# Kernel tuning notes

Hardware: AMD Instinct MI355X
Metric: run time of the kernel (lower is better)

The kernel has to match this reference:

```python
import jax, jax.numpy as jnp
import numpy as np

EMBED_DIM = 2048
NUM_HEADS = 16
NUM_KV_HEADS = 4
KEY_DIM = EMBED_DIM // NUM_HEADS  # 128
B, S = 2, 2048


def setup_inputs() -> dict:
    key = jax.random.key(0)
    ks = jax.random.split(key, 8)
    kv_dim = KEY_DIM * NUM_KV_HEADS
    sc_in = 1.0 / np.sqrt(EMBED_DIM)
    return {
        "query": jax.random.normal(ks[0], (B, S, EMBED_DIM), jnp.float32),
        "key": jax.random.normal(ks[1], (B, S, EMBED_DIM), jnp.float32),
        "value": jax.random.normal(ks[2], (B, S, EMBED_DIM), jnp.float32),
        "mask": jnp.ones((B, S), jnp.float32),
        "Wq": jax.random.normal(ks[3], (EMBED_DIM, EMBED_DIM), jnp.float32) * sc_in,
        "Wk": jax.random.normal(ks[4], (EMBED_DIM, kv_dim), jnp.float32) * sc_in,
        "Wv": jax.random.normal(ks[5], (EMBED_DIM, kv_dim), jnp.float32) * sc_in,
        "Wo": jax.random.normal(ks[6], (EMBED_DIM, EMBED_DIM), jnp.float32) * sc_in,
    }


def reference(query, key, value, mask, Wq, Wk, Wv, Wo):
    b, sq, _ = query.shape
    skv = key.shape[1]
    scale = 1.0 / float(KEY_DIM) ** 0.5
    # projections (no bias)
    q = (query @ Wq).reshape(b, sq, NUM_HEADS, KEY_DIM).transpose(0, 2, 1, 3)      # [B,H,Sq,D]
    k = (key @ Wk).reshape(b, skv, NUM_KV_HEADS, KEY_DIM).transpose(0, 2, 1, 3)    # [B,Hkv,Skv,D]
    v = (value @ Wv).reshape(b, skv, NUM_KV_HEADS, KEY_DIM).transpose(0, 2, 1, 3)  # [B,Hkv,Skv,D]
    n_rep = NUM_HEADS // NUM_KV_HEADS
    k_rep = jnp.repeat(k, n_rep, axis=1)  # [B,H,Skv,D]
    v_rep = jnp.repeat(v, n_rep, axis=1)  # [B,H,Skv,D]
    scores = jnp.einsum("bhqd,bhkd->bhqk", q, k_rep) * scale  # [B,H,Sq,Skv]
    scores = scores + (1.0 - mask[:, None, None, :].astype(scores.dtype)) * -1e9
    attn = jax.nn.softmax(scores, axis=-1)
    out = jnp.einsum("bhqk,bhkd->bhqd", attn, v_rep)  # [B,H,Sq,D]
    out = out.transpose(0, 2, 1, 3).reshape(b, sq, EMBED_DIM)
    return out @ Wo
```

## Files before the change

kernel.cpp:

```cpp
#include <hip/hip_runtime.h>
#include <hip/hip_bf16.h>

#define B_    2
#define S_    2048
#define E_    2048
#define H_    16
#define HKV_  4
#define D_    128
#define NTOK  4096
#define KVDIM 512

typedef __bf16 bf16x8 __attribute__((ext_vector_type(8)));
typedef __bf16 bf16x4 __attribute__((ext_vector_type(4)));
typedef float  f32x4  __attribute__((ext_vector_type(4)));

__device__ __forceinline__ void async_copy16(const void* g, void* l) {
  __builtin_amdgcn_global_load_lds(
      (const __attribute__((address_space(1))) unsigned int*)g,
      (__attribute__((address_space(3))) unsigned int*)l, 16, 0, 0);
}

__global__ __launch_bounds__(256) void transpose_all(
    const float* __restrict__ Wq, const float* __restrict__ Wk,
    const float* __restrict__ Wv, const float* __restrict__ Wo,
    __bf16* __restrict__ WTq, __bf16* __restrict__ WTk,
    __bf16* __restrict__ WTv, __bf16* __restrict__ WoT) {
  const float* in;
  __bf16* out;
  int C;
  switch (blockIdx.z) {
    case 0:  in = Wq; out = WTq; C = E_;   break;
    case 1:  in = Wk; out = WTk; C = KVDIM; break;
    case 2:  in = Wv; out = WTv; C = KVDIM; break;
    default: in = Wo; out = WoT; C = E_;   break;
  }
  const int c0 = blockIdx.x * 32;
  if (c0 >= C) return;
  const int r0 = blockIdx.y * 64;
  __shared__ float t[32][65];
  const int lr = threadIdx.x >> 2;
  const int lc = (threadIdx.x & 3) * 8;
  const float* ip = in + (size_t)(r0 + lr) * C + c0 + lc;
  const f32x4 a0 = *(const f32x4*)ip;
  const f32x4 a1 = *(const f32x4*)(ip + 4);
#pragma unroll
  for (int j = 0; j < 4; ++j) t[lc + j][lr] = a0[j];
#pragma unroll
  for (int j = 0; j < 4; ++j) t[lc + 4 + j][lr] = a1[j];
  __syncthreads();
  const int oc = threadIdx.x >> 3;
  const int orr = (threadIdx.x & 7) * 8;
  bf16x8 v;
#pragma unroll
  for (int j = 0; j < 8; ++j) v[j] = (__bf16)t[oc][orr + j];
  *(bf16x8*)(out + (size_t)(c0 + oc) * E_ + r0 + orr) = v;
}

__global__ __launch_bounds__(256) void convert_q(const float* __restrict__ in,
                                                 __bf16* __restrict__ ob) {
  const size_t i = ((size_t)blockIdx.x * 256 + threadIdx.x) * 8;
  const f32x4 a0 = *(const f32x4*)(in + i);
  const f32x4 a1 = *(const f32x4*)(in + i + 4);
  bf16x8 v;
#pragma unroll
  for (int j = 0; j < 4; ++j) { v[j] = (__bf16)a0[j]; v[4 + j] = (__bf16)a1[j]; }
  *(bf16x8*)(ob + i) = v;
}

__global__ __launch_bounds__(512, 1) void gemm_pipe(
    const __bf16* __restrict__ A, const __bf16* __restrict__ Bt,
    float* __restrict__ Cf, __bf16* __restrict__ Cb, int M, int N, int K,
    int epi) {
  __shared__ __align__(16) __bf16 lds[2 * 24576];

  const int n0 = blockIdx.x * 256;
  const int m0 = blockIdx.y * 128;
  const int tid = threadIdx.x;
  const int w = tid >> 6;
  const int lane = tid & 63;
  const int quad = lane >> 4;
  const int l16 = lane & 15;
  const int wm = w >> 2;
  const int wn = w & 3;
  const int lr = lane >> 3;
  const int ls = lane & 7;

  const __bf16* pa[2];
  const __bf16* pb[4];
#pragma unroll
  for (int r = 0; r < 2; ++r) {
    const int row = r * 64 + w * 8 + lr;
    pa[r] = A + (size_t)(m0 + row) * K + ((ls ^ (row & 7)) * 8);
  }
#pragma unroll
  for (int r = 0; r < 4; ++r) {
    const int row = r * 64 + w * 8 + lr;
    pb[r] = Bt + (size_t)(n0 + row) * K + ((ls ^ (row & 7)) * 8);
  }

  auto stageA = [&](int bufi) {
    __bf16* base = lds + bufi * 24576;
#pragma unroll
    for (int r = 0; r < 2; ++r) {
      async_copy16(pa[r], base + (size_t)(r * 64 + w * 8) * 64);
      pa[r] += 64;
    }
  };
  auto stageB = [&](int bufi) {
    __bf16* base = lds + bufi * 24576 + 8192;
#pragma unroll
    for (int r = 0; r < 4; ++r) {
      async_copy16(pb[r], base + (size_t)(r * 64 + w * 8) * 64);
      pb[r] += 64;
    }
  };

  f32x4 acc[4][4] = {};
  const int NT = K >> 6;
  const int xr = l16 & 7;

  stageA(0);
  stageB(0);
  stageB(1);
  asm volatile("s_waitcnt vmcnt(4)" ::: "memory");
  __builtin_amdgcn_s_barrier();

  for (int t = 0; t < NT; ++t) {
    const __bf16* lA = lds + (t & 1) * 24576;
    const __bf16* lB = lA + 8192;

    bf16x8 af[2][2], bfr[4][2];
#pragma unroll
    for (int f = 0; f < 2; ++f) {
      const int rowb = (wm * 64 + f * 16 + l16) * 64;
#pragma unroll
      for (int ks = 0; ks < 2; ++ks)
        af[f][ks] = *(const bf16x8*)&lA[rowb + (((ks * 4 + quad) ^ xr) * 8)];
    }
#pragma unroll
    for (int g = 0; g < 4; ++g) {
      const int rowb = (wn * 64 + g * 16 + l16) * 64;
#pragma unroll
      for (int ks = 0; ks < 2; ++ks)
        bfr[g][ks] = *(const bf16x8*)&lB[rowb + (((ks * 4 + quad) ^ xr) * 8)];
    }
    if (t + 1 < NT) stageA((t + 1) & 1);
    __builtin_amdgcn_s_barrier();
    asm volatile("s_waitcnt lgkmcnt(0)" ::: "memory");
    __builtin_amdgcn_sched_barrier(0);
    __builtin_amdgcn_s_setprio(1);
#pragma unroll
    for (int f = 0; f < 2; ++f)
#pragma unroll
      for (int g = 0; g < 4; ++g) {
        acc[f][g] = __builtin_amdgcn_mfma_f32_16x16x32_bf16(af[f][0], bfr[g][0],
                                                            acc[f][g], 0, 0, 0);
        acc[f][g] = __builtin_amdgcn_mfma_f32_16x16x32_bf16(af[f][1], bfr[g][1],
                                                            acc[f][g], 0, 0, 0);
      }
    __builtin_amdgcn_s_setprio(0);
    __builtin_amdgcn_s_barrier();

    bf16x8 ah[2][2];
#pragma unroll
    for (int f = 0; f < 2; ++f) {
      const int rowb = (wm * 64 + (f + 2) * 16 + l16) * 64;
#pragma unroll
      for (int ks = 0; ks < 2; ++ks)
        ah[f][ks] = *(const bf16x8*)&lA[rowb + (((ks * 4 + quad) ^ xr) * 8)];
    }
    if (t + 2 < NT) stageB(t & 1);
    __builtin_amdgcn_s_barrier();
    asm volatile("s_waitcnt lgkmcnt(0)" ::: "memory");
    __builtin_amdgcn_sched_barrier(0);
    __builtin_amdgcn_s_setprio(1);
#pragma unroll
    for (int f = 0; f < 2; ++f)
#pragma unroll
      for (int g = 0; g < 4; ++g) {
        acc[f + 2][g] = __builtin_amdgcn_mfma_f32_16x16x32_bf16(
            ah[f][0], bfr[g][0], acc[f + 2][g], 0, 0, 0);
        acc[f + 2][g] = __builtin_amdgcn_mfma_f32_16x16x32_bf16(
            ah[f][1], bfr[g][1], acc[f + 2][g], 0, 0, 0);
      }
    __builtin_amdgcn_s_setprio(0);

    if (t + 2 < NT) {
      asm volatile("s_waitcnt vmcnt(4)" ::: "memory");
      __builtin_amdgcn_s_barrier();
    } else if (t + 1 < NT) {
      asm volatile("s_waitcnt vmcnt(0)" ::: "memory");
      __builtin_amdgcn_s_barrier();
    }
  }

#pragma unroll
  for (int f = 0; f < 4; ++f) {
#pragma unroll
    for (int g = 0; g < 4; ++g) {
#pragma unroll
      for (int r = 0; r < 4; ++r) {
        const int m = m0 + wm * 64 + f * 16 + quad * 4 + r;
        const int n = n0 + wn * 64 + g * 16 + l16;
        if (epi == 0) Cf[(size_t)m * N + n] = acc[f][g][r];
        else          Cb[(size_t)m * N + n] = (__bf16)acc[f][g][r];
      }
    }
  }
}

__global__ __launch_bounds__(256, 2) void gemm_kv(
    const float* __restrict__ key, const float* __restrict__ value,
    const __bf16* __restrict__ WTk, const __bf16* __restrict__ WTv,
    __bf16* __restrict__ Kp, __bf16* __restrict__ Vt) {
  __shared__ __align__(16) __bf16 As[128 * 32];
  __shared__ __align__(16) __bf16 Bs[128 * 32];

  const int bx = blockIdx.x;
  const float* A;
  const __bf16* Bt;
  int n0, epi;
  if (bx < 4) { A = key;   Bt = WTk; n0 = bx * 128;       epi = 0; }
  else        { A = value; Bt = WTv; n0 = (bx - 4) * 128; epi = 1; }
  const int m0 = blockIdx.y * 128;
  const int K = E_;
  const int N = KVDIM;

  const int tid = threadIdx.x;
  const int w = tid >> 6;
  const int lane = tid & 63;
  const int quad = lane >> 4;
  const int l16 = lane & 15;
  const int wr = w >> 1, wc = w & 1;
  const int brow = lane >> 2;
  const int bcol = (lane & 3) * 8;
  const int arow = lane >> 2;
  const int acol = (lane & 3) * 8;

  f32x4 acc[4][4] = {};

  for (int k0 = 0; k0 < K; k0 += 32) {
    __syncthreads();
#pragma unroll
    for (int c = 0; c < 2; ++c) {
      const int chunk = w * 2 + c;
      const int row = chunk * 16 + brow;
      async_copy16(Bt + (size_t)(n0 + row) * K + k0 + bcol, &Bs[chunk * 512]);
    }
#pragma unroll
    for (int s = 0; s < 2; ++s) {
      const int row = w * 32 + s * 16 + arow;
      const float* src = A + (size_t)(m0 + row) * K + k0 + acol;
      const f32x4 a0 = *(const f32x4*)src;
      const f32x4 a1 = *(const f32x4*)(src + 4);
      bf16x8 v;
#pragma unroll
      for (int j = 0; j < 4; ++j) { v[j] = (__bf16)a0[j]; v[4 + j] = (__bf16)a1[j]; }
      *(bf16x8*)&As[row * 32 + acol] = v;
    }
    __syncthreads();
    bf16x8 af[4], bfr[4];
#pragma unroll
    for (int i = 0; i < 4; ++i)
      af[i] = *(const bf16x8*)&As[(wr * 64 + i * 16 + l16) * 32 + quad * 8];
#pragma unroll
    for (int j = 0; j < 4; ++j)
      bfr[j] = *(const bf16x8*)&Bs[(wc * 64 + j * 16 + l16) * 32 + quad * 8];
#pragma unroll
    for (int i = 0; i < 4; ++i)
#pragma unroll
      for (int j = 0; j < 4; ++j)
        acc[i][j] = __builtin_amdgcn_mfma_f32_16x16x32_bf16(af[i], bfr[j],
                                                            acc[i][j], 0, 0, 0);
  }

#pragma unroll
  for (int i = 0; i < 4; ++i) {
#pragma unroll
    for (int j = 0; j < 4; ++j) {
#pragma unroll
      for (int r = 0; r < 4; ++r) {
        const int m = m0 + wr * 64 + i * 16 + quad * 4 + r;
        const int n = n0 + wc * 64 + j * 16 + l16;
        if (epi == 0) {
          Kp[(size_t)m * N + n] = (__bf16)acc[i][j][r];
        } else {
          const int b = m >> 11, s = m & (S_ - 1);
          Vt[((size_t)((b * HKV_ + (n >> 7)) * D_ + (n & (D_ - 1)))) * S_ + s] =
              (__bf16)acc[i][j][r];
        }
      }
    }
  }
}

__global__ __launch_bounds__(256, 2) void attn_kernel(
    const __bf16* __restrict__ Q, const __bf16* __restrict__ Kp,
    const __bf16* __restrict__ Vt, const float* __restrict__ mask,
    __bf16* __restrict__ Oa) {
  __shared__ __align__(16) __bf16 K_lds[64][136];
  __shared__ __align__(16) __bf16 V_lds[128][72];
  __shared__ __align__(16) __bf16 P_lds[4][32][72];

  const int tid = threadIdx.x;
  const int w = tid >> 6, lane = tid & 63, quad = lane >> 4, l16 = lane & 15;
  const int bh = blockIdx.y;
  const int b = bh >> 4, h = bh & 15, hkv = h >> 2;
  const int q0 = blockIdx.x * 128 + w * 32;

  const __bf16* qbase = Q + (size_t)(b * S_ + q0) * E_ + h * D_;
  bf16x8 qf[2][4];
#pragma unroll
  for (int m = 0; m < 2; ++m)
#pragma unroll
    for (int ks = 0; ks < 4; ++ks)
      qf[m][ks] = *(const bf16x8*)(qbase + (size_t)(m * 16 + l16) * E_ +
                                   ks * 32 + quad * 8);

  const __bf16* kbase = Kp + (size_t)(b * S_) * KVDIM + hkv * D_;
  const __bf16* vbase = Vt + (size_t)((b * HKV_ + hkv) * D_) * S_;
  const float* mbase = mask + b * S_;

  const int kr = w * 16 + (lane >> 4);
  const int kc = (lane & 15) * 8;
  const int vr = w * 32 + (lane >> 3);
  const int vc = (lane & 7) * 8;
  const int psw = (quad >> 1) << 5;
  const int pks = l16 >> 3;

  bf16x8 kreg[4], vreg[4];
  float mreg[4];
  auto fetch = [&](int kt) {
#pragma unroll
    for (int i = 0; i < 4; ++i)
      kreg[i] = *(const bf16x8*)(kbase + (size_t)(kt + kr + i * 4) * KVDIM + kc);
#pragma unroll
    for (int i = 0; i < 4; ++i)
      vreg[i] = *(const bf16x8*)(vbase + (size_t)(vr + i * 8) * S_ + kt + vc);
#pragma unroll
    for (int n = 0; n < 4; ++n)
      mreg[n] = mbase[kt + n * 16 + l16];
  };

  f32x4 o[2][8] = {};
  f32x4 lsum[2] = {};
  const float scale = 0.08838834764831845f;

  fetch(0);

  for (int kt = 0; kt < S_; kt += 64) {
#pragma unroll
    for (int i = 0; i < 4; ++i)
      *(bf16x8*)&K_lds[kr + i * 4][kc] = kreg[i];
#pragma unroll
    for (int i = 0; i < 4; ++i)
      *(bf16x8*)&V_lds[vr + i * 8][vc] = vreg[i];
    float bias[4];
#pragma unroll
    for (int n = 0; n < 4; ++n)
      bias[n] = (1.0f - mreg[n]) * -1e9f;
    __syncthreads();

    if (kt + 64 < S_) fetch(kt + 64);

    f32x4 s[2][4] = {};
    __builtin_amdgcn_s_setprio(1);
#pragma unroll
    for (int ks = 0; ks < 4; ++ks) {
#pragma unroll
      for (int n = 0; n < 4; ++n) {
        bf16x8 kf = *(const bf16x8*)&K_lds[n * 16 + l16][ks * 32 + quad * 8];
        s[0][n] = __builtin_amdgcn_mfma_f32_16x16x32_bf16(qf[0][ks], kf,
                                                          s[0][n], 0, 0, 0);
        s[1][n] = __builtin_amdgcn_mfma_f32_16x16x32_bf16(qf[1][ks], kf,
                                                          s[1][n], 0, 0, 0);
      }
    }
    __builtin_amdgcn_s_setprio(0);

#pragma unroll
    for (int m = 0; m < 2; ++m) {
#pragma unroll
      for (int n = 0; n < 4; ++n) {
#pragma unroll
        for (int r = 0; r < 4; ++r) {
          const float p = __expf(s[m][n][r] * scale + bias[n]);
          lsum[m][r] += p;
          P_lds[w][m * 16 + quad * 4 + r][(n * 16 + l16) ^ psw] = (__bf16)p;
        }
      }
    }

    __builtin_amdgcn_s_setprio(1);
#pragma unroll
    for (int ks2 = 0; ks2 < 2; ++ks2) {
      bf16x8 pa[2];
#pragma unroll
      for (int m = 0; m < 2; ++m)
        pa[m] = *(const bf16x8*)
            &P_lds[w][m * 16 + l16][(ks2 ^ pks) * 32 + quad * 8];
#pragma unroll
      for (int dt = 0; dt < 8; ++dt) {
        bf16x8 vf = *(const bf16x8*)&V_lds[dt * 16 + l16][ks2 * 32 + quad * 8];
        o[0][dt] = __builtin_amdgcn_mfma_f32_16x16x32_bf16(pa[0], vf,
                                                           o[0][dt], 0, 0, 0);
        o[1][dt] = __builtin_amdgcn_mfma_f32_16x16x32_bf16(pa[1], vf,
                                                           o[1][dt], 0, 0, 0);
      }
    }
    __builtin_amdgcn_s_setprio(0);

    __syncthreads();
  }

  __bf16* obase = Oa + (size_t)(b * S_ + q0) * E_ + h * D_;
#pragma unroll
  for (int m = 0; m < 2; ++m) {
#pragma unroll
    for (int r = 0; r < 4; ++r) {
      float v = lsum[m][r];
#pragma unroll
      for (int off = 1; off < 16; off <<= 1) v += __shfl_xor(v, off);
      const float inv = 1.0f / v;
#pragma unroll
      for (int dt = 0; dt < 8; ++dt)
        obase[(size_t)(m * 16 + quad * 4 + r) * E_ + dt * 16 + l16] =
            (__bf16)(o[m][dt][r] * inv);
    }
  }
}

extern "C" void kernel_launch(void* const* d_in, const int* in_sizes, int n_in,
                              void* d_out, int out_size, void* d_ws,
                              size_t ws_size, hipStream_t stream) {
  const float* query = (const float*)d_in[0];
  const float* key   = (const float*)d_in[1];
  const float* value = (const float*)d_in[2];
  const float* mask  = (const float*)d_in[3];
  const float* Wq    = (const float*)d_in[4];
  const float* Wk    = (const float*)d_in[5];
  const float* Wv    = (const float*)d_in[6];
  const float* Wo    = (const float*)d_in[7];
  float* out = (float*)d_out;

  __bf16* ws   = (__bf16*)d_ws;
  __bf16* Qp   = ws;
  __bf16* Kp   = Qp + (size_t)NTOK * E_;
  __bf16* Vt   = Kp + (size_t)NTOK * KVDIM;
  __bf16* WoT  = Vt + (size_t)NTOK * KVDIM;
  __bf16* WTq  = WoT + (size_t)E_ * E_;
  __bf16* WTk  = WTq + (size_t)E_ * E_;
  __bf16* WTv  = WTk + (size_t)KVDIM * E_;
  __bf16* Attn = WTq;
  __bf16* qb   = (__bf16*)d_out;

  transpose_all<<<dim3(64, 32, 4), 256, 0, stream>>>(Wq, Wk, Wv, Wo,
                                                     WTq, WTk, WTv, WoT);
  convert_q<<<dim3(4096), 256, 0, stream>>>(query, qb);
  gemm_kv<<<dim3(8, 32), 256, 0, stream>>>(key, value, WTk, WTv, Kp, Vt);
  gemm_pipe<<<dim3(E_ / 256, NTOK / 128), 512, 0, stream>>>(
      qb, WTq, nullptr, Qp, NTOK, E_, E_, 1);
  attn_kernel<<<dim3(S_ / 128, B_ * H_), 256, 0, stream>>>(Qp, Kp, Vt, mask,
                                                           Attn);
  gemm_pipe<<<dim3(E_ / 256, NTOK / 128), 512, 0, stream>>>(
      Attn, WoT, out, nullptr, NTOK, E_, E_, 0);
}
```

Measured before the change: 404.2 us.

## Pre-convert K/V inputs to bf16, remap GEMM blocks per XCD, simplify attention

Folds the query/key/value fp32→bf16 conversions into the transpose launch, so gemm_kv can load its A tiles with async global→LDS copies instead of converting in registers. Both GEMMs switch to a 1D grid whose block index is remapped so neighbouring tiles land on the same XCD, aiming for better L2 reuse. In attention, the mask is no longer prefetched into registers, and the P_lds XOR swizzle is dropped. These trade extra global traffic for the bf16 key/value copies and a possible return of LDS bank conflicts on P against lower register pressure and simpler addressing.

```diff
diff --git a/kernel.cpp b/kernel.cpp
--- a/kernel.cpp
+++ b/kernel.cpp
@@ -24,7 +24,34 @@
     const float* __restrict__ Wq, const float* __restrict__ Wk,
     const float* __restrict__ Wv, const float* __restrict__ Wo,
     __bf16* __restrict__ WTq, __bf16* __restrict__ WTk,
-    __bf16* __restrict__ WTv, __bf16* __restrict__ WoT) {
+    __bf16* __restrict__ WTv, __bf16* __restrict__ WoT,
+    const float* __restrict__ query, const float* __restrict__ key,
+    const float* __restrict__ value, __bf16* __restrict__ qb,
+    __bf16* __restrict__ kb, __bf16* __restrict__ vb) {
+  if (blockIdx.z >= 4) {
+    const float* src;
+    __bf16* dst;
+    switch (blockIdx.z) {
+      case 4:  src = query; dst = qb; break;
+      case 5:  src = key;   dst = kb; break;
+      default: src = value; dst = vb; break;
+    }
+    const size_t i =
+        (((size_t)blockIdx.y * 64 + blockIdx.x) * 256 + threadIdx.x) * 16;
+    const f32x4 a0 = *(const f32x4*)(src + i);
+    const f32x4 a1 = *(const f32x4*)(src + i + 4);
+    const f32x4 a2 = *(const f32x4*)(src + i + 8);
+    const f32x4 a3 = *(const f32x4*)(src + i + 12);
+    bf16x8 v0, v1;
+#pragma unroll
+    for (int j = 0; j < 4; ++j) {
+      v0[j] = (__bf16)a0[j]; v0[4 + j] = (__bf16)a1[j];
+      v1[j] = (__bf16)a2[j]; v1[4 + j] = (__bf16)a3[j];
+    }
+    *(bf16x8*)(dst + i) = v0;
+    *(bf16x8*)(dst + i + 8) = v1;
+    return;
+  }
   const float* in;
   __bf16* out;
   int C;
@@ -56,25 +83,17 @@
   *(bf16x8*)(out + (size_t)(c0 + oc) * E_ + r0 + orr) = v;
 }
 
-__global__ __launch_bounds__(256) void convert_q(const float* __restrict__ in,
-                                                 __bf16* __restrict__ ob) {
-  const size_t i = ((size_t)blockIdx.x * 256 + threadIdx.x) * 8;
-  const f32x4 a0 = *(const f32x4*)(in + i);
-  const f32x4 a1 = *(const f32x4*)(in + i + 4);
-  bf16x8 v;
-#pragma unroll
-  for (int j = 0; j < 4; ++j) { v[j] = (__bf16)a0[j]; v[4 + j] = (__bf16)a1[j]; }
-  *(bf16x8*)(ob + i) = v;
-}
-
 __global__ __launch_bounds__(512, 1) void gemm_pipe(
     const __bf16* __restrict__ A, const __bf16* __restrict__ Bt,
     float* __restrict__ Cf, __bf16* __restrict__ Cb, int M, int N, int K,
     int epi) {
   __shared__ __align__(16) __bf16 lds[2 * 24576];
 
-  const int n0 = blockIdx.x * 256;
-  const int m0 = blockIdx.y * 128;
+  const int bxl = blockIdx.x;
+  const int xcd = bxl & 7;
+  const int sub = bxl >> 3;
+  const int m0 = ((xcd >> 1) * 8 + (sub >> 2)) * 128;
+  const int n0 = ((xcd & 1) * 4 + (sub & 3)) * 256;
   const int tid = threadIdx.x;
   const int w = tid >> 6;
   const int lane = tid & 63;
@@ -210,19 +229,20 @@
 }
 
 __global__ __launch_bounds__(256, 2) void gemm_kv(
-    const float* __restrict__ key, const float* __restrict__ value,
+    const __bf16* __restrict__ kb, const __bf16* __restrict__ vb,
     const __bf16* __restrict__ WTk, const __bf16* __restrict__ WTv,
     __bf16* __restrict__ Kp, __bf16* __restrict__ Vt) {
   __shared__ __align__(16) __bf16 As[128 * 32];
   __shared__ __align__(16) __bf16 Bs[128 * 32];
 
-  const int bx = blockIdx.x;
-  const float* A;
-  const __bf16* Bt;
-  int n0, epi;
-  if (bx < 4) { A = key;   Bt = WTk; n0 = bx * 128;       epi = 0; }
-  else        { A = value; Bt = WTv; n0 = (bx - 4) * 128; epi = 1; }
-  const int m0 = blockIdx.y * 128;
+  const int bxl = blockIdx.x;
+  const int xcd = bxl & 7;
+  const int sub = bxl >> 3;
+  const int mat = xcd & 1;
+  const int m0 = ((xcd >> 1) * 8 + (sub >> 2)) * 128;
+  const int n0 = (sub & 3) * 128;
+  const __bf16* A  = mat ? vb : kb;
+  const __bf16* Bt = mat ? WTv : WTk;
   const int K = E_;
   const int N = KVDIM;
 
@@ -234,8 +254,6 @@
   const int wr = w >> 1, wc = w & 1;
   const int brow = lane >> 2;
   const int bcol = (lane & 3) * 8;
-  const int arow = lane >> 2;
-  const int acol = (lane & 3) * 8;
 
   f32x4 acc[4][4] = {};
 
@@ -246,17 +264,7 @@
       const int chunk = w * 2 + c;
       const int row = chunk * 16 + brow;
       async_copy16(Bt + (size_t)(n0 + row) * K + k0 + bcol, &Bs[chunk * 512]);
-    }
-#pragma unroll
-    for (int s = 0; s < 2; ++s) {
-      const int row = w * 32 + s * 16 + arow;
-      const float* src = A + (size_t)(m0 + row) * K + k0 + acol;
-      const f32x4 a0 = *(const f32x4*)src;
-      const f32x4 a1 = *(const f32x4*)(src + 4);
-      bf16x8 v;
-#pragma unroll
-      for (int j = 0; j < 4; ++j) { v[j] = (__bf16)a0[j]; v[4 + j] = (__bf16)a1[j]; }
-      *(bf16x8*)&As[row * 32 + acol] = v;
+      async_copy16(A + (size_t)(m0 + row) * K + k0 + bcol, &As[chunk * 512]);
     }
     __syncthreads();
     bf16x8 af[4], bfr[4];
@@ -282,7 +290,7 @@
       for (int r = 0; r < 4; ++r) {
         const int m = m0 + wr * 64 + i * 16 + quad * 4 + r;
         const int n = n0 + wc * 64 + j * 16 + l16;
-        if (epi == 0) {
+        if (mat == 0) {
           Kp[(size_t)m * N + n] = (__bf16)acc[i][j][r];
         } else {
           const int b = m >> 11, s = m & (S_ - 1);
@@ -325,11 +333,8 @@
   const int kc = (lane & 15) * 8;
   const int vr = w * 32 + (lane >> 3);
   const int vc = (lane & 7) * 8;
-  const int psw = (quad >> 1) << 5;
-  const int pks = l16 >> 3;
 
   bf16x8 kreg[4], vreg[4];
-  float mreg[4];
   auto fetch = [&](int kt) {
 #pragma unroll
     for (int i = 0; i < 4; ++i)
@@ -337,9 +342,6 @@
 #pragma unroll
     for (int i = 0; i < 4; ++i)
       vreg[i] = *(const bf16x8*)(vbase + (size_t)(vr + i * 8) * S_ + kt + vc);
-#pragma unroll
-    for (int n = 0; n < 4; ++n)
-      mreg[n] = mbase[kt + n * 16 + l16];
   };
 
   f32x4 o[2][8] = {};
@@ -355,10 +357,6 @@
 #pragma unroll
     for (int i = 0; i < 4; ++i)
       *(bf16x8*)&V_lds[vr + i * 8][vc] = vreg[i];
-    float bias[4];
-#pragma unroll
-    for (int n = 0; n < 4; ++n)
-      bias[n] = (1.0f - mreg[n]) * -1e9f;
     __syncthreads();
 
     if (kt + 64 < S_) fetch(kt + 64);
@@ -378,6 +376,10 @@
     }
     __builtin_amdgcn_s_setprio(0);
 
+    float bias[4];
+#pragma unroll
+    for (int n = 0; n < 4; ++n)
+      bias[n] = (1.0f - mbase[kt + n * 16 + l16]) * -1e9f;
 #pragma unroll
     for (int m = 0; m < 2; ++m) {
 #pragma unroll
@@ -386,7 +388,7 @@
         for (int r = 0; r < 4; ++r) {
           const float p = __expf(s[m][n][r] * scale + bias[n]);
           lsum[m][r] += p;
-          P_lds[w][m * 16 + quad * 4 + r][(n * 16 + l16) ^ psw] = (__bf16)p;
+          P_lds[w][m * 16 + quad * 4 + r][n * 16 + l16] = (__bf16)p;
         }
       }
     }
@@ -397,8 +399,7 @@
       bf16x8 pa[2];
 #pragma unroll
       for (int m = 0; m < 2; ++m)
-        pa[m] = *(const bf16x8*)
-            &P_lds[w][m * 16 + l16][(ks2 ^ pks) * 32 + quad * 8];
+        pa[m] = *(const bf16x8*)&P_lds[w][m * 16 + l16][ks2 * 32 + quad * 8];
 #pragma unroll
       for (int dt = 0; dt < 8; ++dt) {
         bf16x8 vf = *(const bf16x8*)&V_lds[dt * 16 + l16][ks2 * 32 + quad * 8];
@@ -453,15 +454,16 @@
   __bf16* WTv  = WTk + (size_t)KVDIM * E_;
   __bf16* Attn = WTq;
   __bf16* qb   = (__bf16*)d_out;
-
-  transpose_all<<<dim3(64, 32, 4), 256, 0, stream>>>(Wq, Wk, Wv, Wo,
-                                                     WTq, WTk, WTv, WoT);
-  convert_q<<<dim3(4096), 256, 0, stream>>>(query, qb);
-  gemm_kv<<<dim3(8, 32), 256, 0, stream>>>(key, value, WTk, WTv, Kp, Vt);
-  gemm_pipe<<<dim3(E_ / 256, NTOK / 128), 512, 0, stream>>>(
+  __bf16* kb   = qb + (size_t)NTOK * E_;
+  __bf16* vb   = Qp;
+
+  transpose_all<<<dim3(64, 32, 7), 256, 0, stream>>>(
+      Wq, Wk, Wv, Wo, WTq, WTk, WTv, WoT, query, key, value, qb, kb, vb);
+  gemm_kv<<<dim3(256), 256, 0, stream>>>(kb, vb, WTk, WTv, Kp, Vt);
+  gemm_pipe<<<dim3(256), 512, 0, stream>>>(
       qb, WTq, nullptr, Qp, NTOK, E_, E_, 1);
   attn_kernel<<<dim3(S_ / 128, B_ * H_), 256, 0, stream>>>(Qp, Kp, Vt, mask,
                                                            Attn);
-  gemm_pipe<<<dim3(E_ / 256, NTOK / 128), 512, 0, stream>>>(
+  gemm_pipe<<<dim3(256), 512, 0, stream>>>(
       Attn, WoT, out, nullptr, NTOK, E_, E_, 0);
 }
```

Measured after the change: 381.2 us. 1.06x faster.
